# Optimization experiments

Hardware: AMD Instinct MI355X
Metric: run time of the kernel (lower is better)

The kernel has to match this reference:

```python
import jax, jax.numpy as jnp
import numpy as np
import math

SLIDING_WINDOW = 1024  # matches init kwarg

def setup_inputs() -> dict:
    key = jax.random.key(0)
    ks = jax.random.split(key, 6)
    B, S, Hq, Hkv, D = 1, 2048, 32, 8, 128
    NUM_PAGES, STRIDE = 300, 16
    q = jax.random.normal(ks[0], (B, S, Hq, D), dtype=jnp.float32)
    k = jax.random.normal(ks[1], (B, S, Hkv, D), dtype=jnp.float32)
    v = jax.random.normal(ks[2], (B, S, Hkv, D), dtype=jnp.float32)
    sink = jax.random.normal(ks[3], (Hq,), dtype=jnp.float32)
    cache_state = jnp.zeros((NUM_PAGES, STRIDE, 2, Hkv, D), dtype=jnp.float32)
    seq_block_ids = jax.random.randint(ks[4], (B, S // STRIDE), 0, NUM_PAGES, dtype=jnp.int64)
    return {"q": q, "k": k, "v": v, "sink": sink,
            "cache_state": cache_state, "seq_block_ids": seq_block_ids}


def reference(q, k, v, sink, cache_state, seq_block_ids):
    B, S, Hq, D = q.shape
    Hkv = k.shape[2]
    stride = cache_state.shape[1]

    # --- paged cache write (prefill side effect) ---
    kv = jnp.stack([k, v], axis=2)                       # [B,S,2,Hkv,D]
    pages = kv.reshape(B * (S // stride), stride, 2, Hkv, D)
    _ = cache_state.at[seq_block_ids.reshape(-1)].set(pages)

    # --- decomposed attention: matmul + mask + softmax(+sink) + matmul ---
    rep = Hq // Hkv
    ke = jnp.repeat(k, rep, axis=2)                      # [B,S,Hq,D] (GQA expand)
    ve = jnp.repeat(v, rep, axis=2)
    scale = 1.0 / math.sqrt(D)
    scores = jnp.einsum('bihd,bjhd->bhij', q, ke) * scale  # [B,Hq,S,S]

    i = jnp.arange(S)[:, None]
    j = jnp.arange(S)[None, :]
    allowed = (j <= i) & (i - j < SLIDING_WINDOW)        # causal + sliding window
    neg = jnp.finfo(scores.dtype).min
    logits = jnp.where(allowed, scores, neg)

    # attention sink: extra per-head logit appended; contributes to denominator only
    sink_l = jnp.broadcast_to(sink[None, :, None, None], (B, Hq, S, 1))
    probs = jax.nn.softmax(jnp.concatenate([logits, sink_l], axis=-1), axis=-1)[..., :S]

    out = jnp.einsum('bhij,bjhd->bihd', probs, ve)       # [B,S,Hq,D]
    return out
```

## Files before the change

kernel.cpp:

```cpp
#include <hip/hip_runtime.h>
#include <hip/hip_bf16.h>


#define S_LEN 2048
#define DH    128
#define HQ    32
#define HKV   8
#define WIN   1024
#define BR    64
#define BC    32
#define NT    (S_LEN / BC)
#define FM    16.0f
#define TILE_CH 512

typedef unsigned short u16;
typedef __attribute__((ext_vector_type(8))) short  short8;
typedef __attribute__((ext_vector_type(4))) float  floatx4;
typedef __attribute__((ext_vector_type(4))) unsigned int uintx4;

__device__ __forceinline__ unsigned rne1(float a) {
    unsigned u = __float_as_uint(a);
    return (u + 0x7FFFu + ((u >> 16) & 1u)) >> 16;
}
__device__ __forceinline__ unsigned rne_pk(float a, float b) {
    return rne1(a) | (rne1(b) << 16);
}

__global__ __launch_bounds__(256) void pack_kv(const float* __restrict__ kg,
                                               const float* __restrict__ vg,
                                               u16* __restrict__ kp,
                                               u16* __restrict__ vtp)
{
    __shared__ float Vs[BC][DH + 1];
    const int b   = blockIdx.x;
    const int hk  = b >> 6;
    const int jt  = b & 63;
    const int tid = threadIdx.x;
    const int j0  = jt * BC;

    #pragma unroll
    for (int t = 0; t < 4; t++) {
        int idx = tid + t * 256;
        int j   = idx >> 5;
        int dc  = idx & 31;
        floatx4 f = *(const floatx4*)(vg + ((size_t)(j0 + j) * HKV + hk) * DH + dc * 4);
        Vs[j][dc * 4 + 0] = f[0]; Vs[j][dc * 4 + 1] = f[1];
        Vs[j][dc * 4 + 2] = f[2]; Vs[j][dc * 4 + 3] = f[3];
    }

    u16* kpt = kp + (size_t)b * TILE_CH * 8;
    #pragma unroll
    for (int t = 0; t < 2; t++) {
        int c = tid + t * 256;
        int row = c >> 4, cc = c & 15;
        const float* p = kg + ((size_t)(j0 + row) * HKV + hk) * DH + cc * 8;
        floatx4 f0 = *(const floatx4*)p;
        floatx4 f1 = *(const floatx4*)(p + 4);
        int pc = (row << 4) | (cc ^ (row & 7));
        *(uintx4*)(kpt + pc * 8) =
            (uintx4){rne_pk(f0[0], f0[1]), rne_pk(f0[2], f0[3]),
                     rne_pk(f1[0], f1[1]), rne_pk(f1[2], f1[3])};
    }
    __syncthreads();

    u16* vpt = vtp + (size_t)b * TILE_CH * 8;
    #pragma unroll
    for (int t = 0; t < 2; t++) {
        int q  = tid + t * 256;
        int dd = q >> 2, c = q & 3;
        unsigned w0 = rne_pk(Vs[c * 4 + 0][dd], Vs[c * 4 + 16][dd]);
        unsigned w1 = rne_pk(Vs[c * 4 + 1][dd], Vs[c * 4 + 17][dd]);
        unsigned w2 = rne_pk(Vs[c * 4 + 2][dd], Vs[c * 4 + 18][dd]);
        unsigned w3 = rne_pk(Vs[c * 4 + 3][dd], Vs[c * 4 + 19][dd]);
        int qp = (dd << 2) | (c ^ ((dd >> 2) & 3));
        *(uintx4*)(vpt + qp * 8) = (uintx4){w0, w1, w2, w3};
    }
}

__launch_bounds__(256, 4)
__global__ void fa_kernel(const float* __restrict__ qg,
                          const u16* __restrict__ kp,
                          const u16* __restrict__ vtp,
                          const float* __restrict__ sg,
                          float* __restrict__ outg)
{
    __shared__ __align__(16) u16 Kt[2][TILE_CH * 8];
    __shared__ __align__(16) u16 Vt[2][TILE_CH * 8];
    __shared__ __align__(16) u16 Pb[BR * 40];

    const int tid  = threadIdx.x;
    const int w    = tid >> 6;
    const int lane = tid & 63;
    const int quad = lane >> 4;
    const int l16  = lane & 15;

    const int bid  = blockIdx.x;
    const int hk   = bid & 7;
    const int idx  = bid >> 3;
    const int hrem = idx & 3;
    const int u5   = (idx >> 2) & 7;
    const int t4   = idx >> 5;
    const int qbt[4] = {u5, 15 - u5, 16 + u5, 31 - u5};
    const int qb   = qbt[t4];
    const int h    = hk * 4 + hrem;

    const int i0 = qb * BR;
    const int m0 = i0 + w * 16;

    short8 qf[4];
    {
        const float* qrow = qg + ((size_t)(m0 + l16) * HQ + h) * DH;
        #pragma unroll
        for (int kk = 0; kk < 4; kk++) {
            const float* p = qrow + kk * 32 + quad * 8;
            floatx4 f0 = *(const floatx4*)p;
            floatx4 f1 = *(const floatx4*)(p + 4);
            uintx4 u = (uintx4){rne_pk(f0[0], f0[1]), rne_pk(f0[2], f0[3]),
                                rne_pk(f1[0], f1[1]), rne_pk(f1[2], f1[3])};
            qf[kk] = *(short8*)&u;
        }
    }

    floatx4 acc[8];
    #pragma unroll
    for (int i = 0; i < 8; i++) acc[i] = (floatx4){0.f, 0.f, 0.f, 0.f};
    float l_part[4] = {0.f, 0.f, 0.f, 0.f};

    int c_r[4];
    #pragma unroll
    for (int r = 0; r < 4; r++) c_r[r] = m0 + quad * 4 + r - l16;

    int jlo = i0 - (WIN - 1); if (jlo < 0) jlo = 0;
    const int jt_lo = jlo >> 5;
    const int jt_hi = (i0 + BR - 1) >> 5;

    const float SC2 = 0.08838834764831845f * 1.4426950408889634f;

    const int ch0 = w * 64 + lane;
    auto stage = [&](int bb, int jt) {
        const u16* kpt = kp  + ((size_t)(hk * NT + jt)) * TILE_CH * 8;
        const u16* vpt = vtp + ((size_t)(hk * NT + jt)) * TILE_CH * 8;
        #pragma unroll
        for (int it = 0; it < 2; it++) {
            int ch = ch0 + it * 256;
            __builtin_amdgcn_global_load_lds(
                (const __attribute__((address_space(1))) unsigned*)(kpt + ch * 8),
                (__attribute__((address_space(3))) unsigned*)(&Kt[bb][ch * 8]), 16, 0, 0);
            __builtin_amdgcn_global_load_lds(
                (const __attribute__((address_space(1))) unsigned*)(vpt + ch * 8),
                (__attribute__((address_space(3))) unsigned*)(&Vt[bb][ch * 8]), 16, 0, 0);
        }
    };

    stage(0, jt_lo);
    int bb = 0;

    for (int jt = jt_lo; jt <= jt_hi; jt++) {
        const int j0 = jt << 5;

        __syncthreads();

        if (jt < jt_hi) stage(bb ^ 1, jt + 1);

        floatx4 sc[2];
        sc[0] = (floatx4){0.f, 0.f, 0.f, 0.f};
        sc[1] = (floatx4){0.f, 0.f, 0.f, 0.f};
        #pragma unroll
        for (int kk = 0; kk < 4; kk++) {
            #pragma unroll
            for (int n = 0; n < 2; n++) {
                int row = n * 16 + l16;
                int cc  = kk * 4 + quad;
                int pc  = (row << 4) | (cc ^ (row & 7));
                short8 kf = *(const short8*)(&Kt[bb][pc * 8]);
                sc[n] = __builtin_amdgcn_mfma_f32_16x16x32_bf16(qf[kk], kf, sc[n], 0, 0, 0);
            }
        }

        const int prow0 = w * 16 + quad * 4;
        const bool interior = (j0 + (BC - 1) <= i0) && (j0 >= i0 + BR - WIN);
        if (interior) {
            #pragma unroll
            for (int r = 0; r < 4; r++) {
                float p0 = exp2f(fmaf(sc[0][r], SC2, -FM));
                float p1 = exp2f(fmaf(sc[1][r], SC2, -FM));
                l_part[r] += p0 + p1;
                *(unsigned*)(&Pb[(prow0 + r) * 40 + l16 * 2]) = rne_pk(p0, p1);
            }
        } else {
            #pragma unroll
            for (int r = 0; r < 4; r++) {
                bool a0 = (j0 <= c_r[r]) && (j0 > c_r[r] - WIN);
                bool a1 = (j0 + 16 <= c_r[r]) && (j0 + 16 > c_r[r] - WIN);
                float p0 = a0 ? exp2f(fmaf(sc[0][r], SC2, -FM)) : 0.f;
                float p1 = a1 ? exp2f(fmaf(sc[1][r], SC2, -FM)) : 0.f;
                l_part[r] += p0 + p1;
                *(unsigned*)(&Pb[(prow0 + r) * 40 + l16 * 2]) = rne_pk(p0, p1);
            }
        }

        {
            short8 pf = *(const short8*)(&Pb[(w * 16 + l16) * 40 + quad * 8]);
            #pragma unroll
            for (int nf = 0; nf < 8; nf++) {
                int dd = nf * 16 + l16;
                int qp = (dd << 2) | (quad ^ ((dd >> 2) & 3));
                short8 vf = *(const short8*)(&Vt[bb][qp * 8]);
                acc[nf] = __builtin_amdgcn_mfma_f32_16x16x32_bf16(pf, vf, acc[nf], 0, 0, 0);
            }
        }
        bb ^= 1;
    }

    const float sk2 = exp2f(fmaf(sg[h], 1.4426950408889634f, -FM));
    float inv[4];
    #pragma unroll
    for (int r = 0; r < 4; r++) {
        float l = l_part[r];
        #pragma unroll
        for (int off = 1; off < 16; off <<= 1)
            l += __shfl_xor(l, off);
        inv[r] = 1.f / (l + sk2);
    }
    #pragma unroll
    for (int nf = 0; nf < 8; nf++) {
        int d = nf * 16 + l16;
        #pragma unroll
        for (int r = 0; r < 4; r++) {
            int ig = m0 + quad * 4 + r;
            outg[((size_t)ig * HQ + h) * DH + d] = acc[nf][r] * inv[r];
        }
    }
}

__launch_bounds__(256, 4)
__global__ void fa_fallback(const float* __restrict__ qg,
                            const float* __restrict__ kg,
                            const float* __restrict__ vg,
                            const float* __restrict__ sg,
                            float* __restrict__ outg)
{
    __shared__ __align__(16) u16 Kt[BC * DH];
    __shared__ __align__(16) u16 Vt[DH * BC];
    __shared__ __align__(16) u16 Pb[BR * 40];

    const int tid  = threadIdx.x;
    const int w    = tid >> 6;
    const int lane = tid & 63;
    const int quad = lane >> 4;
    const int l16  = lane & 15;

    const int qb = blockIdx.x / HQ;
    const int h  = blockIdx.x % HQ;
    const int hk = h >> 2;
    const int i0 = qb * BR;
    const int m0 = i0 + w * 16;

    short8 qf[4];
    {
        const float* qrow = qg + ((size_t)(m0 + l16) * HQ + h) * DH;
        #pragma unroll
        for (int kk = 0; kk < 4; kk++) {
            const float* p = qrow + kk * 32 + quad * 8;
            floatx4 f0 = *(const floatx4*)p;
            floatx4 f1 = *(const floatx4*)(p + 4);
            uintx4 u = (uintx4){rne_pk(f0[0], f0[1]), rne_pk(f0[2], f0[3]),
                                rne_pk(f1[0], f1[1]), rne_pk(f1[2], f1[3])};
            qf[kk] = *(short8*)&u;
        }
    }

    floatx4 acc[8];
    #pragma unroll
    for (int i = 0; i < 8; i++) acc[i] = (floatx4){0.f, 0.f, 0.f, 0.f};
    float l_part[4] = {0.f, 0.f, 0.f, 0.f};

    int jlo = i0 - (WIN - 1); if (jlo < 0) jlo = 0;
    const int jt_lo = jlo >> 5;
    const int jt_hi = (i0 + BR - 1) >> 5;
    const float SC2 = 0.08838834764831845f * 1.4426950408889634f;

    for (int jt = jt_lo; jt <= jt_hi; jt++) {
        const int j0 = jt << 5;
        __syncthreads();
        #pragma unroll
        for (int it = 0; it < 2; it++) {
            int g   = tid + 256 * it;
            int row = g >> 4, cc = g & 15;
            int pc  = (row << 4) | (cc ^ (row & 7));
            const float* kpp = kg + ((size_t)(j0 + row) * HKV + hk) * DH + cc * 8;
            floatx4 f0 = *(const floatx4*)kpp;
            floatx4 f1 = *(const floatx4*)(kpp + 4);
            *(uintx4*)(&Kt[pc * 8]) =
                (uintx4){rne_pk(f0[0], f0[1]), rne_pk(f0[2], f0[3]),
                         rne_pk(f1[0], f1[1]), rne_pk(f1[2], f1[3])};
        }
        #pragma unroll
        for (int it = 0; it < 2; it++) {
            int g  = tid + 256 * it;
            int d  = g & 127, jc = g >> 7;
            const float* vp = vg + ((size_t)(j0 + jc * 8) * HKV + hk) * DH + d;
            float e0 = vp[0 * HKV * DH], e1 = vp[1 * HKV * DH];
            float e2 = vp[2 * HKV * DH], e3 = vp[3 * HKV * DH];
            float e4 = vp[4 * HKV * DH], e5 = vp[5 * HKV * DH];
            float e6 = vp[6 * HKV * DH], e7 = vp[7 * HKV * DH];
            int pc = (d << 2) | (jc ^ ((d >> 2) & 3));
            *(uintx4*)(&Vt[pc * 8]) =
                (uintx4){rne_pk(e0, e1), rne_pk(e2, e3), rne_pk(e4, e5), rne_pk(e6, e7)};
        }
        __syncthreads();

        floatx4 sc[2];
        sc[0] = (floatx4){0.f, 0.f, 0.f, 0.f};
        sc[1] = (floatx4){0.f, 0.f, 0.f, 0.f};
        #pragma unroll
        for (int kk = 0; kk < 4; kk++) {
            #pragma unroll
            for (int n = 0; n < 2; n++) {
                int row = n * 16 + l16;
                int cc  = kk * 4 + quad;
                int pc  = (row << 4) | (cc ^ (row & 7));
                short8 kf = *(const short8*)(&Kt[pc * 8]);
                sc[n] = __builtin_amdgcn_mfma_f32_16x16x32_bf16(qf[kk], kf, sc[n], 0, 0, 0);
            }
        }
        #pragma unroll
        for (int r = 0; r < 4; r++) {
            int   i_g = m0 + quad * 4 + r;
            int   jg0 = j0 + l16, jg1 = j0 + 16 + l16;
            bool  a0  = (jg0 <= i_g) && (i_g - jg0 < WIN);
            bool  a1  = (jg1 <= i_g) && (i_g - jg1 < WIN);
            float p0  = a0 ? exp2f(fmaf(sc[0][r], SC2, -FM)) : 0.f;
            float p1  = a1 ? exp2f(fmaf(sc[1][r], SC2, -FM)) : 0.f;
            l_part[r] += p0 + p1;
            int prow = w * 16 + quad * 4 + r;
            *(unsigned*)(&Pb[prow * 40 + 2 * l16]) = rne_pk(p0, p1);
        }
        {
            short8 pf = *(const short8*)(&Pb[(w * 16 + l16) * 40 + quad * 8]);
            #pragma unroll
            for (int nf = 0; nf < 8; nf++) {
                int dd = nf * 16 + l16;
                int qp = (dd << 2) | (quad ^ ((dd >> 2) & 3));
                short8 vf = *(const short8*)(&Vt[qp * 8]);
                acc[nf] = __builtin_amdgcn_mfma_f32_16x16x32_bf16(pf, vf, acc[nf], 0, 0, 0);
            }
        }
    }

    const float sk2 = exp2f(fmaf(sg[h], 1.4426950408889634f, -FM));
    float inv[4];
    #pragma unroll
    for (int r = 0; r < 4; r++) {
        float l = l_part[r];
        #pragma unroll
        for (int off = 1; off < 16; off <<= 1)
            l += __shfl_xor(l, off);
        inv[r] = 1.f / (l + sk2);
    }
    #pragma unroll
    for (int nf = 0; nf < 8; nf++) {
        int d = nf * 16 + l16;
        #pragma unroll
        for (int r = 0; r < 4; r++) {
            int ig = m0 + quad * 4 + r;
            outg[((size_t)ig * HQ + h) * DH + d] = acc[nf][r] * inv[r];
        }
    }
}

extern "C" void kernel_launch(void* const* d_in, const int* in_sizes, int n_in,
                              void* d_out, int out_size, void* d_ws, size_t ws_size,
                              hipStream_t stream) {
    const float* q  = (const float*)d_in[0];
    const float* k  = (const float*)d_in[1];
    const float* v  = (const float*)d_in[2];
    const float* sk = (const float*)d_in[3];
    float* out = (float*)d_out;

    const size_t tile_elems = (size_t)HKV * NT * TILE_CH * 8;
    const size_t need = 2 * tile_elems * sizeof(u16);

    if (ws_size >= need) {
        u16* kp  = (u16*)d_ws;
        u16* vtp = kp + tile_elems;
        pack_kv<<<dim3(HKV * NT), 256, 0, stream>>>(k, v, kp, vtp);
        fa_kernel<<<dim3((S_LEN / BR) * HQ), 256, 0, stream>>>(q, kp, vtp, sk, out);
    } else {
        fa_fallback<<<dim3((S_LEN / BR) * HQ), 256, 0, stream>>>(q, k, v, sk, out);
    }
}
```

Measured before the change: 163.1 us.

## Give each wave two 16-row query tiles with 128-thread blocks; use hardware bf16 convert

The flash-attention kernel now runs 2 waves per block, and each wave handles 32 query rows as two 16-row MFMA tiles. Each K and V fragment read from LDS therefore feeds two MFMAs, halving LDS fragment traffic per unit of compute. Software round-to-nearest bf16 packing of Q and P is replaced by the v_cvt_pk_bf16_f32 instruction. The cost is roughly double the accumulator registers per thread, fewer waves per block, and more staging work per thread, which may reduce occupancy and latency hiding.

```diff
diff --git a/kernel.cpp b/kernel.cpp
--- a/kernel.cpp
+++ b/kernel.cpp
@@ -24,6 +24,11 @@
 }
 __device__ __forceinline__ unsigned rne_pk(float a, float b) {
     return rne1(a) | (rne1(b) << 16);
+}
+__device__ __forceinline__ unsigned cvt_pk(float a, float b) {
+    unsigned r;
+    asm("v_cvt_pk_bf16_f32 %0, %1, %2" : "=v"(r) : "v"(a), "v"(b));
+    return r;
 }
 
 __global__ __launch_bounds__(256) void pack_kv(const float* __restrict__ kg,
@@ -77,7 +82,7 @@
     }
 }
 
-__launch_bounds__(256, 4)
+__launch_bounds__(128, 2)
 __global__ void fa_kernel(const float* __restrict__ qg,
                           const u16* __restrict__ kp,
                           const u16* __restrict__ vtp,
@@ -105,30 +110,36 @@
     const int h    = hk * 4 + hrem;
 
     const int i0 = qb * BR;
-    const int m0 = i0 + w * 16;
-
-    short8 qf[4];
-    {
-        const float* qrow = qg + ((size_t)(m0 + l16) * HQ + h) * DH;
+    const int m0 = i0 + w * 32;
+
+    short8 qf[2][4];
+    #pragma unroll
+    for (int m = 0; m < 2; m++) {
+        const float* qrow = qg + ((size_t)(m0 + m * 16 + l16) * HQ + h) * DH;
         #pragma unroll
         for (int kk = 0; kk < 4; kk++) {
             const float* p = qrow + kk * 32 + quad * 8;
             floatx4 f0 = *(const floatx4*)p;
             floatx4 f1 = *(const floatx4*)(p + 4);
-            uintx4 u = (uintx4){rne_pk(f0[0], f0[1]), rne_pk(f0[2], f0[3]),
-                                rne_pk(f1[0], f1[1]), rne_pk(f1[2], f1[3])};
-            qf[kk] = *(short8*)&u;
-        }
-    }
-
-    floatx4 acc[8];
-    #pragma unroll
-    for (int i = 0; i < 8; i++) acc[i] = (floatx4){0.f, 0.f, 0.f, 0.f};
-    float l_part[4] = {0.f, 0.f, 0.f, 0.f};
-
-    int c_r[4];
-    #pragma unroll
-    for (int r = 0; r < 4; r++) c_r[r] = m0 + quad * 4 + r - l16;
+            uintx4 u = (uintx4){cvt_pk(f0[0], f0[1]), cvt_pk(f0[2], f0[3]),
+                                cvt_pk(f1[0], f1[1]), cvt_pk(f1[2], f1[3])};
+            qf[m][kk] = *(short8*)&u;
+        }
+    }
+
+    floatx4 acc[2][8];
+    #pragma unroll
+    for (int m = 0; m < 2; m++)
+        #pragma unroll
+        for (int i = 0; i < 8; i++) acc[m][i] = (floatx4){0.f, 0.f, 0.f, 0.f};
+    float l_part[2][4] = {{0.f, 0.f, 0.f, 0.f}, {0.f, 0.f, 0.f, 0.f}};
+
+    int c_r[2][4];
+    #pragma unroll
+    for (int m = 0; m < 2; m++)
+        #pragma unroll
+        for (int r = 0; r < 4; r++)
+            c_r[m][r] = m0 + m * 16 + quad * 4 + r - l16;
 
     int jlo = i0 - (WIN - 1); if (jlo < 0) jlo = 0;
     const int jt_lo = jlo >> 5;
@@ -136,13 +147,12 @@
 
     const float SC2 = 0.08838834764831845f * 1.4426950408889634f;
 
-    const int ch0 = w * 64 + lane;
     auto stage = [&](int bb, int jt) {
         const u16* kpt = kp  + ((size_t)(hk * NT + jt)) * TILE_CH * 8;
         const u16* vpt = vtp + ((size_t)(hk * NT + jt)) * TILE_CH * 8;
         #pragma unroll
-        for (int it = 0; it < 2; it++) {
-            int ch = ch0 + it * 256;
+        for (int it = 0; it < 4; it++) {
+            int ch = tid + it * 128;
             __builtin_amdgcn_global_load_lds(
                 (const __attribute__((address_space(1))) unsigned*)(kpt + ch * 8),
                 (__attribute__((address_space(3))) unsigned*)(&Kt[bb][ch * 8]), 16, 0, 0);
@@ -162,75 +172,94 @@
 
         if (jt < jt_hi) stage(bb ^ 1, jt + 1);
 
-        floatx4 sc[2];
-        sc[0] = (floatx4){0.f, 0.f, 0.f, 0.f};
-        sc[1] = (floatx4){0.f, 0.f, 0.f, 0.f};
+        floatx4 sc[2][2];
+        #pragma unroll
+        for (int m = 0; m < 2; m++) {
+            sc[m][0] = (floatx4){0.f, 0.f, 0.f, 0.f};
+            sc[m][1] = (floatx4){0.f, 0.f, 0.f, 0.f};
+        }
         #pragma unroll
         for (int kk = 0; kk < 4; kk++) {
-            #pragma unroll
-            for (int n = 0; n < 2; n++) {
-                int row = n * 16 + l16;
-                int cc  = kk * 4 + quad;
-                int pc  = (row << 4) | (cc ^ (row & 7));
-                short8 kf = *(const short8*)(&Kt[bb][pc * 8]);
-                sc[n] = __builtin_amdgcn_mfma_f32_16x16x32_bf16(qf[kk], kf, sc[n], 0, 0, 0);
-            }
-        }
-
-        const int prow0 = w * 16 + quad * 4;
+            const int cc = kk * 4 + quad;
+            const int row0 = l16;
+            const int row1 = 16 + l16;
+            const int pc0 = (row0 << 4) | (cc ^ (row0 & 7));
+            const int pc1 = (row1 << 4) | (cc ^ (row1 & 7));
+            short8 kf0 = *(const short8*)(&Kt[bb][pc0 * 8]);
+            short8 kf1 = *(const short8*)(&Kt[bb][pc1 * 8]);
+            sc[0][0] = __builtin_amdgcn_mfma_f32_16x16x32_bf16(qf[0][kk], kf0, sc[0][0], 0, 0, 0);
+            sc[1][0] = __builtin_amdgcn_mfma_f32_16x16x32_bf16(qf[1][kk], kf0, sc[1][0], 0, 0, 0);
+            sc[0][1] = __builtin_amdgcn_mfma_f32_16x16x32_bf16(qf[0][kk], kf1, sc[0][1], 0, 0, 0);
+            sc[1][1] = __builtin_amdgcn_mfma_f32_16x16x32_bf16(qf[1][kk], kf1, sc[1][1], 0, 0, 0);
+        }
+
         const bool interior = (j0 + (BC - 1) <= i0) && (j0 >= i0 + BR - WIN);
         if (interior) {
             #pragma unroll
-            for (int r = 0; r < 4; r++) {
-                float p0 = exp2f(fmaf(sc[0][r], SC2, -FM));
-                float p1 = exp2f(fmaf(sc[1][r], SC2, -FM));
-                l_part[r] += p0 + p1;
-                *(unsigned*)(&Pb[(prow0 + r) * 40 + l16 * 2]) = rne_pk(p0, p1);
+            for (int m = 0; m < 2; m++) {
+                const int prow0 = w * 32 + m * 16 + quad * 4;
+                #pragma unroll
+                for (int r = 0; r < 4; r++) {
+                    float p0 = exp2f(fmaf(sc[m][0][r], SC2, -FM));
+                    float p1 = exp2f(fmaf(sc[m][1][r], SC2, -FM));
+                    l_part[m][r] += p0 + p1;
+                    *(unsigned*)(&Pb[(prow0 + r) * 40 + l16 * 2]) = cvt_pk(p0, p1);
+                }
             }
         } else {
             #pragma unroll
-            for (int r = 0; r < 4; r++) {
-                bool a0 = (j0 <= c_r[r]) && (j0 > c_r[r] - WIN);
-                bool a1 = (j0 + 16 <= c_r[r]) && (j0 + 16 > c_r[r] - WIN);
-                float p0 = a0 ? exp2f(fmaf(sc[0][r], SC2, -FM)) : 0.f;
-                float p1 = a1 ? exp2f(fmaf(sc[1][r], SC2, -FM)) : 0.f;
-                l_part[r] += p0 + p1;
-                *(unsigned*)(&Pb[(prow0 + r) * 40 + l16 * 2]) = rne_pk(p0, p1);
+            for (int m = 0; m < 2; m++) {
+                const int prow0 = w * 32 + m * 16 + quad * 4;
+                #pragma unroll
+                for (int r = 0; r < 4; r++) {
+                    bool a0 = (j0 <= c_r[m][r]) && (j0 > c_r[m][r] - WIN);
+                    bool a1 = (j0 + 16 <= c_r[m][r]) && (j0 + 16 > c_r[m][r] - WIN);
+                    float p0 = a0 ? exp2f(fmaf(sc[m][0][r], SC2, -FM)) : 0.f;
+                    float p1 = a1 ? exp2f(fmaf(sc[m][1][r], SC2, -FM)) : 0.f;
+                    l_part[m][r] += p0 + p1;
+                    *(unsigned*)(&Pb[(prow0 + r) * 40 + l16 * 2]) = cvt_pk(p0, p1);
+                }
             }
         }
 
         {
-            short8 pf = *(const short8*)(&Pb[(w * 16 + l16) * 40 + quad * 8]);
+            short8 pf0 = *(const short8*)(&Pb[(w * 32 + l16) * 40 + quad * 8]);
+            short8 pf1 = *(const short8*)(&Pb[(w * 32 + 16 + l16) * 40 + quad * 8]);
             #pragma unroll
             for (int nf = 0; nf < 8; nf++) {
                 int dd = nf * 16 + l16;
                 int qp = (dd << 2) | (quad ^ ((dd >> 2) & 3));
                 short8 vf = *(const short8*)(&Vt[bb][qp * 8]);
-                acc[nf] = __builtin_amdgcn_mfma_f32_16x16x32_bf16(pf, vf, acc[nf], 0, 0, 0);
+                acc[0][nf] = __builtin_amdgcn_mfma_f32_16x16x32_bf16(pf0, vf, acc[0][nf], 0, 0, 0);
+                acc[1][nf] = __builtin_amdgcn_mfma_f32_16x16x32_bf16(pf1, vf, acc[1][nf], 0, 0, 0);
             }
         }
         bb ^= 1;
     }
 
     const float sk2 = exp2f(fmaf(sg[h], 1.4426950408889634f, -FM));
-    float inv[4];
-    #pragma unroll
-    for (int r = 0; r < 4; r++) {
-        float l = l_part[r];
-        #pragma unroll
-        for (int off = 1; off < 16; off <<= 1)
-            l += __shfl_xor(l, off);
-        inv[r] = 1.f / (l + sk2);
-    }
-    #pragma unroll
-    for (int nf = 0; nf < 8; nf++) {
-        int d = nf * 16 + l16;
+    float inv[2][4];
+    #pragma unroll
+    for (int m = 0; m < 2; m++)
         #pragma unroll
         for (int r = 0; r < 4; r++) {
-            int ig = m0 + quad * 4 + r;
-            outg[((size_t)ig * HQ + h) * DH + d] = acc[nf][r] * inv[r];
-        }
-    }
+            float l = l_part[m][r];
+            #pragma unroll
+            for (int off = 1; off < 16; off <<= 1)
+                l += __shfl_xor(l, off);
+            inv[m][r] = 1.f / (l + sk2);
+        }
+    #pragma unroll
+    for (int m = 0; m < 2; m++)
+        #pragma unroll
+        for (int nf = 0; nf < 8; nf++) {
+            int d = nf * 16 + l16;
+            #pragma unroll
+            for (int r = 0; r < 4; r++) {
+                int ig = m0 + m * 16 + quad * 4 + r;
+                outg[((size_t)ig * HQ + h) * DH + d] = acc[m][nf][r] * inv[m][r];
+            }
+        }
 }
 
 __launch_bounds__(256, 4)
@@ -385,7 +414,7 @@
         u16* kp  = (u16*)d_ws;
         u16* vtp = kp + tile_elems;
         pack_kv<<<dim3(HKV * NT), 256, 0, stream>>>(k, v, kp, vtp);
-        fa_kernel<<<dim3((S_LEN / BR) * HQ), 256, 0, stream>>>(q, kp, vtp, sk, out);
+        fa_kernel<<<dim3((S_LEN / BR) * HQ), 128, 0, stream>>>(q, kp, vtp, sk, out);
     } else {
         fa_fallback<<<dim3((S_LEN / BR) * HQ), 256, 0, stream>>>(q, k, v, sk, out);
     }
```

Result: slower. 170.2 us (+4.4%).

## Process two heads per 512-thread block sharing staged KV tiles

Applied to the files above, without the earlier changes.

Doubles the block to 512 threads, with each block handling two query heads that share one KV head. The K/V tiles staged into LDS are reused by both heads, and the grid shrinks to 512 blocks with a simpler causal load-balancing map. It also swaps the manual bf16 rounding for the hardware v_cvt_pk_bf16_f32 instruction and raises wave priority around the MFMA loops. The trade-off is more waves per block and fewer blocks, which changes occupancy and the load balance across CUs.

```diff
diff --git a/kernel.cpp b/kernel.cpp
--- a/kernel.cpp
+++ b/kernel.cpp
@@ -24,6 +24,11 @@
 }
 __device__ __forceinline__ unsigned rne_pk(float a, float b) {
     return rne1(a) | (rne1(b) << 16);
+}
+__device__ __forceinline__ unsigned cvt_pk(float a, float b) {
+    unsigned r;
+    asm("v_cvt_pk_bf16_f32 %0, %1, %2" : "=v"(r) : "v"(a), "v"(b));
+    return r;
 }
 
 __global__ __launch_bounds__(256) void pack_kv(const float* __restrict__ kg,
@@ -77,7 +82,7 @@
     }
 }
 
-__launch_bounds__(256, 4)
+__launch_bounds__(512, 4)
 __global__ void fa_kernel(const float* __restrict__ qg,
                           const u16* __restrict__ kp,
                           const u16* __restrict__ vtp,
@@ -86,7 +91,7 @@
 {
     __shared__ __align__(16) u16 Kt[2][TILE_CH * 8];
     __shared__ __align__(16) u16 Vt[2][TILE_CH * 8];
-    __shared__ __align__(16) u16 Pb[BR * 40];
+    __shared__ __align__(16) u16 Pb[8 * 16 * 40];
 
     const int tid  = threadIdx.x;
     const int w    = tid >> 6;
@@ -96,16 +101,13 @@
 
     const int bid  = blockIdx.x;
     const int hk   = bid & 7;
-    const int idx  = bid >> 3;
-    const int hrem = idx & 3;
-    const int u5   = (idx >> 2) & 7;
-    const int t4   = idx >> 5;
-    const int qbt[4] = {u5, 15 - u5, 16 + u5, 31 - u5};
-    const int qb   = qbt[t4];
-    const int h    = hk * 4 + hrem;
-
-    const int i0 = qb * BR;
-    const int m0 = i0 + w * 16;
+    const int j    = bid >> 3;
+    const int hp   = j >> 5;
+    const int u    = j & 31;
+    const int qb   = hp ? (31 - u) : u;
+    const int h    = hk * 4 + hp * 2 + (w & 1);
+    const int i0   = qb * BR;
+    const int m0   = i0 + (w >> 1) * 16;
 
     short8 qf[4];
     {
@@ -115,9 +117,9 @@
             const float* p = qrow + kk * 32 + quad * 8;
             floatx4 f0 = *(const floatx4*)p;
             floatx4 f1 = *(const floatx4*)(p + 4);
-            uintx4 u = (uintx4){rne_pk(f0[0], f0[1]), rne_pk(f0[2], f0[3]),
-                                rne_pk(f1[0], f1[1]), rne_pk(f1[2], f1[3])};
-            qf[kk] = *(short8*)&u;
+            uintx4 uq = (uintx4){cvt_pk(f0[0], f0[1]), cvt_pk(f0[2], f0[3]),
+                                 cvt_pk(f1[0], f1[1]), cvt_pk(f1[2], f1[3])};
+            qf[kk] = *(short8*)&uq;
         }
     }
 
@@ -136,20 +138,16 @@
 
     const float SC2 = 0.08838834764831845f * 1.4426950408889634f;
 
-    const int ch0 = w * 64 + lane;
     auto stage = [&](int bb, int jt) {
         const u16* kpt = kp  + ((size_t)(hk * NT + jt)) * TILE_CH * 8;
         const u16* vpt = vtp + ((size_t)(hk * NT + jt)) * TILE_CH * 8;
-        #pragma unroll
-        for (int it = 0; it < 2; it++) {
-            int ch = ch0 + it * 256;
-            __builtin_amdgcn_global_load_lds(
-                (const __attribute__((address_space(1))) unsigned*)(kpt + ch * 8),
-                (__attribute__((address_space(3))) unsigned*)(&Kt[bb][ch * 8]), 16, 0, 0);
-            __builtin_amdgcn_global_load_lds(
-                (const __attribute__((address_space(1))) unsigned*)(vpt + ch * 8),
-                (__attribute__((address_space(3))) unsigned*)(&Vt[bb][ch * 8]), 16, 0, 0);
-        }
+        int ch = tid;
+        __builtin_amdgcn_global_load_lds(
+            (const __attribute__((address_space(1))) unsigned*)(kpt + ch * 8),
+            (__attribute__((address_space(3))) unsigned*)(&Kt[bb][ch * 8]), 16, 0, 0);
+        __builtin_amdgcn_global_load_lds(
+            (const __attribute__((address_space(1))) unsigned*)(vpt + ch * 8),
+            (__attribute__((address_space(3))) unsigned*)(&Vt[bb][ch * 8]), 16, 0, 0);
     };
 
     stage(0, jt_lo);
@@ -165,6 +163,7 @@
         floatx4 sc[2];
         sc[0] = (floatx4){0.f, 0.f, 0.f, 0.f};
         sc[1] = (floatx4){0.f, 0.f, 0.f, 0.f};
+        __builtin_amdgcn_s_setprio(1);
         #pragma unroll
         for (int kk = 0; kk < 4; kk++) {
             #pragma unroll
@@ -176,6 +175,7 @@
                 sc[n] = __builtin_amdgcn_mfma_f32_16x16x32_bf16(qf[kk], kf, sc[n], 0, 0, 0);
             }
         }
+        __builtin_amdgcn_s_setprio(0);
 
         const int prow0 = w * 16 + quad * 4;
         const bool interior = (j0 + (BC - 1) <= i0) && (j0 >= i0 + BR - WIN);
@@ -185,7 +185,7 @@
                 float p0 = exp2f(fmaf(sc[0][r], SC2, -FM));
                 float p1 = exp2f(fmaf(sc[1][r], SC2, -FM));
                 l_part[r] += p0 + p1;
-                *(unsigned*)(&Pb[(prow0 + r) * 40 + l16 * 2]) = rne_pk(p0, p1);
+                *(unsigned*)(&Pb[(prow0 + r) * 40 + l16 * 2]) = cvt_pk(p0, p1);
             }
         } else {
             #pragma unroll
@@ -195,12 +195,13 @@
                 float p0 = a0 ? exp2f(fmaf(sc[0][r], SC2, -FM)) : 0.f;
                 float p1 = a1 ? exp2f(fmaf(sc[1][r], SC2, -FM)) : 0.f;
                 l_part[r] += p0 + p1;
-                *(unsigned*)(&Pb[(prow0 + r) * 40 + l16 * 2]) = rne_pk(p0, p1);
+                *(unsigned*)(&Pb[(prow0 + r) * 40 + l16 * 2]) = cvt_pk(p0, p1);
             }
         }
 
         {
             short8 pf = *(const short8*)(&Pb[(w * 16 + l16) * 40 + quad * 8]);
+            __builtin_amdgcn_s_setprio(1);
             #pragma unroll
             for (int nf = 0; nf < 8; nf++) {
                 int dd = nf * 16 + l16;
@@ -208,6 +209,7 @@
                 short8 vf = *(const short8*)(&Vt[bb][qp * 8]);
                 acc[nf] = __builtin_amdgcn_mfma_f32_16x16x32_bf16(pf, vf, acc[nf], 0, 0, 0);
             }
+            __builtin_amdgcn_s_setprio(0);
         }
         bb ^= 1;
     }
@@ -385,7 +387,7 @@
         u16* kp  = (u16*)d_ws;
         u16* vtp = kp + tile_elems;
         pack_kv<<<dim3(HKV * NT), 256, 0, stream>>>(k, v, kp, vtp);
-        fa_kernel<<<dim3((S_LEN / BR) * HQ), 256, 0, stream>>>(q, kp, vtp, sk, out);
+        fa_kernel<<<dim3(512), 512, 0, stream>>>(q, kp, vtp, sk, out);
     } else {
         fa_fallback<<<dim3((S_LEN / BR) * HQ), 256, 0, stream>>>(q, k, v, sk, out);
     }
```

Measured after the change: 165.4 us. Within noise of the previous version (+1.4%).

## Load V fragments directly from global into registers and use hardware bf16 pack

Applied to the files above, without the earlier changes.

Removes the LDS staging buffer for V and has each lane load its V fragments straight from global memory into registers at the start of each tile, with the offsets precomputed once. This frees LDS, which may raise occupancy, and removes the LDS write/read traffic for V. The cost is that V loads are no longer coalesced through the async global-to-LDS path, each wave re-reads V from global/L2, and the loads are issued only one tile ahead of use. Software round-to-nearest-even bf16 packing is also replaced with the v_cvt_pk_bf16_f32 instruction.

```diff
diff --git a/kernel.cpp b/kernel.cpp
--- a/kernel.cpp
+++ b/kernel.cpp
@@ -24,6 +24,11 @@
 }
 __device__ __forceinline__ unsigned rne_pk(float a, float b) {
     return rne1(a) | (rne1(b) << 16);
+}
+__device__ __forceinline__ unsigned cvt_pk(float a, float b) {
+    unsigned r;
+    asm("v_cvt_pk_bf16_f32 %0, %1, %2" : "=v"(r) : "v"(a), "v"(b));
+    return r;
 }
 
 __global__ __launch_bounds__(256) void pack_kv(const float* __restrict__ kg,
@@ -85,7 +90,6 @@
                           float* __restrict__ outg)
 {
     __shared__ __align__(16) u16 Kt[2][TILE_CH * 8];
-    __shared__ __align__(16) u16 Vt[2][TILE_CH * 8];
     __shared__ __align__(16) u16 Pb[BR * 40];
 
     const int tid  = threadIdx.x;
@@ -115,10 +119,17 @@
             const float* p = qrow + kk * 32 + quad * 8;
             floatx4 f0 = *(const floatx4*)p;
             floatx4 f1 = *(const floatx4*)(p + 4);
-            uintx4 u = (uintx4){rne_pk(f0[0], f0[1]), rne_pk(f0[2], f0[3]),
-                                rne_pk(f1[0], f1[1]), rne_pk(f1[2], f1[3])};
-            qf[kk] = *(short8*)&u;
-        }
+            uintx4 uq = (uintx4){cvt_pk(f0[0], f0[1]), cvt_pk(f0[2], f0[3]),
+                                 cvt_pk(f1[0], f1[1]), cvt_pk(f1[2], f1[3])};
+            qf[kk] = *(short8*)&uq;
+        }
+    }
+
+    int voff[8];
+    #pragma unroll
+    for (int nf = 0; nf < 8; nf++) {
+        int dd = nf * 16 + l16;
+        voff[nf] = ((dd << 2) | (quad ^ ((dd >> 2) & 3))) * 8;
     }
 
     floatx4 acc[8];
@@ -136,19 +147,17 @@
 
     const float SC2 = 0.08838834764831845f * 1.4426950408889634f;
 
+    const u16* vbase = vtp + (((size_t)hk * NT) << 12);
+
     const int ch0 = w * 64 + lane;
     auto stage = [&](int bb, int jt) {
-        const u16* kpt = kp  + ((size_t)(hk * NT + jt)) * TILE_CH * 8;
-        const u16* vpt = vtp + ((size_t)(hk * NT + jt)) * TILE_CH * 8;
+        const u16* kpt = kp + ((size_t)(hk * NT + jt)) * TILE_CH * 8;
         #pragma unroll
         for (int it = 0; it < 2; it++) {
             int ch = ch0 + it * 256;
             __builtin_amdgcn_global_load_lds(
                 (const __attribute__((address_space(1))) unsigned*)(kpt + ch * 8),
                 (__attribute__((address_space(3))) unsigned*)(&Kt[bb][ch * 8]), 16, 0, 0);
-            __builtin_amdgcn_global_load_lds(
-                (const __attribute__((address_space(1))) unsigned*)(vpt + ch * 8),
-                (__attribute__((address_space(3))) unsigned*)(&Vt[bb][ch * 8]), 16, 0, 0);
         }
     };
 
@@ -159,6 +168,14 @@
         const int j0 = jt << 5;
 
         __syncthreads();
+
+        short8 vf[8];
+        {
+            const u16* vt = vbase + ((size_t)jt << 12);
+            #pragma unroll
+            for (int nf = 0; nf < 8; nf++)
+                vf[nf] = *(const short8*)(vt + voff[nf]);
+        }
 
         if (jt < jt_hi) stage(bb ^ 1, jt + 1);
 
@@ -185,7 +202,7 @@
                 float p0 = exp2f(fmaf(sc[0][r], SC2, -FM));
                 float p1 = exp2f(fmaf(sc[1][r], SC2, -FM));
                 l_part[r] += p0 + p1;
-                *(unsigned*)(&Pb[(prow0 + r) * 40 + l16 * 2]) = rne_pk(p0, p1);
+                *(unsigned*)(&Pb[(prow0 + r) * 40 + l16 * 2]) = cvt_pk(p0, p1);
             }
         } else {
             #pragma unroll
@@ -195,7 +212,7 @@
                 float p0 = a0 ? exp2f(fmaf(sc[0][r], SC2, -FM)) : 0.f;
                 float p1 = a1 ? exp2f(fmaf(sc[1][r], SC2, -FM)) : 0.f;
                 l_part[r] += p0 + p1;
-                *(unsigned*)(&Pb[(prow0 + r) * 40 + l16 * 2]) = rne_pk(p0, p1);
+                *(unsigned*)(&Pb[(prow0 + r) * 40 + l16 * 2]) = cvt_pk(p0, p1);
             }
         }
 
@@ -203,10 +220,7 @@
             short8 pf = *(const short8*)(&Pb[(w * 16 + l16) * 40 + quad * 8]);
             #pragma unroll
             for (int nf = 0; nf < 8; nf++) {
-                int dd = nf * 16 + l16;
-                int qp = (dd << 2) | (quad ^ ((dd >> 2) & 3));
-                short8 vf = *(const short8*)(&Vt[bb][qp * 8]);
-                acc[nf] = __builtin_amdgcn_mfma_f32_16x16x32_bf16(pf, vf, acc[nf], 0, 0, 0);
+                acc[nf] = __builtin_amdgcn_mfma_f32_16x16x32_bf16(pf, vf[nf], acc[nf], 0, 0, 0);
             }
         }
         bb ^= 1;
```

After: 174.5 us. +7.0%, slower.
